# Performance work log

Hardware: AMD Instinct MI355X
Metric: run time of the kernel (lower is better)

Reference implementation:

```python
import jax, jax.numpy as jnp
import numpy as np

NEG = -10000.0
SINK = 16  # first 16 keys are always-attended sink tokens


def setup_inputs() -> dict:
    key = jax.random.key(0)
    k0, k1, k2 = jax.random.split(key, 3)
    B, H, KH, S, D = 1, 16, 4, 2048, 128
    return {
        "query": jax.random.normal(k0, (B, H, S, D), dtype=jnp.float32),
        "key_t": jax.random.normal(k1, (B, KH, S, D), dtype=jnp.float32),
        "value": jax.random.normal(k2, (B, KH, S, D), dtype=jnp.float32),
        "lsh_threshold": jnp.full((KH,), 70.0, dtype=jnp.float32),
        "top_k": 64,
        "window_size": 128,
    }


def reference(query, key_t, value, lsh_threshold, top_k, window_size):
    # query: [B,H,S,D]; key_t/value: [B,KH,S,D] (GQA, QH = H//KH)
    B, H, S, D = query.shape
    KH = key_t.shape[1]
    QH = H // KH
    q = query.reshape(B, KH, QH, S, D)

    # LSH sign-bit matching count. packbits64(x>=0) + (D - xor_popcount) ==
    # number of positions where sign(q)==sign(k) == (D + <sgn(q),sgn(k)>)/2.
    qs = jnp.where(q >= 0, 1.0, -1.0).astype(jnp.float32)
    ksgn = jnp.where(key_t >= 0, 1.0, -1.0).astype(jnp.float32)
    match = (D + jnp.einsum('bkqsd,bkld->bkqsl', qs, ksgn)) * 0.5  # [B,KH,QH,S,S]
    # max over the QH group (dim=2, keepdim) then compare against per-KV-head threshold
    lsh_mask = match.max(axis=2, keepdims=True) > lsh_threshold.reshape(1, KH, 1, 1, 1)

    qi = jnp.arange(S)[:, None]
    ki = jnp.arange(S)[None, :]
    causal = qi >= ki                                             # [S,S]
    window = ((jnp.abs(qi - ki) < window_size) | (ki < SINK)) & causal

    mask = causal & lsh_mask                                      # [B,KH,QH,S,S]

    scale = 1.0 / jnp.sqrt(jnp.asarray(D, jnp.float32))
    scores = jnp.einsum('bkqsd,bkld->bkqsl', q, key_t) * scale    # [B,KH,QH,S,S]
    scores = jnp.where(jnp.logical_not(mask) & jnp.logical_not(window), NEG, scores)

    # long-term candidates: exclude the local window, then take top_k per query row
    scores_lt = jnp.where(window, NEG, scores)
    _, idx = jax.lax.top_k(scores_lt, top_k)                      # [B,KH,QH,S,top_k]
    topk_mask = jnp.put_along_axis(
        jnp.zeros(scores.shape, dtype=bool), idx, True, axis=-1, inplace=False)

    both = window | topk_mask
    probs = jax.nn.softmax(jnp.where(both, scores, NEG), axis=-1)
    out = jnp.einsum('bkqsl,bkld->bskqd', probs, value)           # [B,S,KH,QH,D]
    return out.reshape(B, S, H * D)
```

## Files before the change

### kernel.cpp

```cpp
#include <hip/hip_runtime.h>

#define S_LEN   2048
#define D_DIM   128
#define KH_N    4
#define QH_N    4
#define H_N     (KH_N * QH_N)
#define SINK_N  16
#define MAXW    160
#define MAXC    1904
#define MAXT    2048
#define NREG    16
#define CHUNK   512
#define MAXSEL  208
#define PLANE32 676

typedef __attribute__((ext_vector_type(8))) _Float16 f16x8;
typedef __attribute__((ext_vector_type(2))) _Float16 f16x2;
typedef __attribute__((ext_vector_type(4))) float f32x4;

__device__ __forceinline__ void lds_fence() {
  asm volatile("s_waitcnt lgkmcnt(0)" ::: "memory");
}
__device__ __forceinline__ unsigned short f2h(float f) {
  _Float16 h = (_Float16)f;
  return __builtin_bit_cast(unsigned short, h);
}
__device__ __forceinline__ unsigned int pkrtz_u32(float a, float b) {
  return __builtin_bit_cast(unsigned int, __builtin_amdgcn_cvt_pkrtz(a, b));
}
__device__ __forceinline__ unsigned int pack_okey16(float a, float b) {
  unsigned int u = pkrtz_u32(a, b);
  unsigned int t = (u >> 15) & 0x00010001u;
  return u ^ ((t * 0x7FFFu) | 0x80008000u);
}
__device__ __forceinline__ float okinv16(unsigned int k) {
  unsigned short bits = (k & 0x8000u) ? (unsigned short)(k & 0x7FFFu)
                                      : (unsigned short)(~k & 0xFFFFu);
  return (float)__builtin_bit_cast(_Float16, bits);
}

__global__ __launch_bounds__(256) void pack_kernel(
    const float* __restrict__ k, const float* __restrict__ v,
    unsigned long long* __restrict__ signs,
    unsigned short* __restrict__ kf16, unsigned int* __restrict__ vf16) {
  const int wid  = (blockIdx.x * 256 + threadIdx.x) >> 6;
  const int lane = threadIdx.x & 63;
  const int rbase = wid * 4;
  const int KROWS = KH_N * S_LEN;

  if (rbase < KROWS) {
    const float* src = k + (size_t)rbase * D_DIM;
    float a[4], b[4];
#pragma unroll
    for (int r = 0; r < 4; r++) {
      a[r] = src[r * D_DIM + lane];
      b[r] = src[r * D_DIM + 64 + lane];
    }
#pragma unroll
    for (int r = 0; r < 4; r++) {
      unsigned long long b0 = __ballot(a[r] >= 0.0f);
      unsigned long long b1 = __ballot(b[r] >= 0.0f);
      if (lane == 0) {
        signs[(size_t)(rbase + r) * 2]     = b0;
        signs[(size_t)(rbase + r) * 2 + 1] = b1;
      }
      unsigned short* rb = kf16 + (size_t)(rbase + r) * 128;
      rb[lane]      = f2h(a[r]);
      rb[64 + lane] = f2h(b[r]);
    }
  } else {
    int vr = rbase - KROWS;
    const float* src = v + (size_t)vr * D_DIM;
    float2 f2[4];
#pragma unroll
    for (int r = 0; r < 4; r++)
      f2[r] = *(const float2*)(src + r * D_DIM + lane * 2);
#pragma unroll
    for (int r = 0; r < 4; r++) {
      unsigned int pk = (unsigned int)f2h(f2[r].x) |
                        ((unsigned int)f2h(f2[r].y) << 16);
      vf16[(size_t)(vr + r) * 64 + lane] = pk;
    }
  }
}

__global__ __launch_bounds__(256, 5) void attn_kernel(
    const float* __restrict__ query, const float* __restrict__ thr,
    const int* __restrict__ p_topk, const int* __restrict__ p_wsz,
    const unsigned long long* __restrict__ signs,
    const unsigned short* __restrict__ kf16,
    const unsigned int* __restrict__ vf16,
    float* __restrict__ out) {
  const int xcd  = blockIdx.x & 7;
  const int kh   = xcd >> 1;
  const int s    = (S_LEN - 1) - (((blockIdx.x >> 3) << 1) | (xcd & 1));
  const int tid  = threadIdx.x;
  const int lane = tid & 63;
  const int qh   = tid >> 6;
  const int col  = lane & 15;
  const int quad = lane >> 4;

  __shared__ __align__(16) unsigned int buf[QH_N * PLANE32];
  __shared__ __align__(16) unsigned short q_f16[QH_N][136];
  __shared__ unsigned short idx_sh[MAXT];
  __shared__ unsigned long long qs_sh[QH_N][2];
  __shared__ int ncand_sh;

  const int   topk   = *p_topk;
  const int   wsz    = *p_wsz;
  const float thresh = thr[kh];
  const float scale  = 0.088388347648318447f;

  {
    int h0 = tid >> 7, d = tid & 127;
    float f0 = query[((size_t)(kh * QH_N + h0) * S_LEN + s) * D_DIM + d];
    float f1 = query[((size_t)(kh * QH_N + h0 + 2) * S_LEN + s) * D_DIM + d];
    unsigned long long b0 = __ballot(f0 >= 0.0f);
    unsigned long long b1 = __ballot(f1 >= 0.0f);
    if (lane == 0) {
      qs_sh[qh >> 1][qh & 1] = b0;
      qs_sh[2 + (qh >> 1)][qh & 1] = b1;
    }
    q_f16[h0][d]     = f2h(f0 * scale);
    q_f16[h0 + 2][d] = f2h(f1 * scale);
  }
  if (tid == 0) ncand_sh = 0;

  int wlo = s - (wsz - 1); if (wlo < 0) wlo = 0;
  int nsink = wlo < SINK_N ? wlo : SINK_N;
  int nw = nsink + (s - wlo + 1);
  if (nw > MAXW) nw = MAXW;
  for (int e = tid; e < nw; e += 256)
    idx_sh[e] = (unsigned short)(e < nsink ? e : wlo + (e - nsink));
  __syncthreads();

  unsigned long long qs0[QH_N], qs1[QH_N];
#pragma unroll
  for (int h = 0; h < QH_N; h++) { qs0[h] = qs_sh[h][0]; qs1[h] = qs_sh[h][1]; }
  const unsigned long long* ksg = signs + (size_t)kh * S_LEN * 2;
  int lt_hi = s - wsz;
  for (int l0 = SINK_N; l0 <= lt_hi; l0 += 256) {
    int l = l0 + tid;
    bool match = false;
    if (l <= lt_hi) {
      ulonglong2 kk = *(const ulonglong2*)(ksg + 2 * l);
      int best = 0;
#pragma unroll
      for (int h = 0; h < QH_N; h++) {
        int m = 128 - __popcll(qs0[h] ^ kk.x) - __popcll(qs1[h] ^ kk.y);
        best = best > m ? best : m;
      }
      match = ((float)best > thresh);
    }
    unsigned long long m = __ballot(match);
    if (m) {
      int base = 0;
      if (lane == 0) base = atomicAdd(&ncand_sh, __popcll(m));
      base = __shfl(base, 0);
      if (match) {
        int pos = base + __popcll(m & ((1ull << lane) - 1ull));
        if (pos < MAXC) idx_sh[nw + pos] = (unsigned short)l;
      }
    }
  }
  __syncthreads();
  int nc = ncand_sh < MAXC ? ncand_sh : MAXC;
  int ntot = nw + nc;
  int ntot_pad = (ntot + 15) & ~15;
  for (int i = ntot + tid; i < ntot_pad; i += 256) idx_sh[i] = 0;
  __syncthreads();

  f16x8 bfrag[4];
  f16x8 bzero = {0, 0, 0, 0, 0, 0, 0, 0};
#pragma unroll
  for (int ks = 0; ks < 4; ks++)
    bfrag[ks] = (col < 4) ? *(const f16x8*)&q_f16[col][ks * 32 + quad * 8] : bzero;

  const unsigned short* kf_h = kf16 + ((size_t)kh << 11) * 128;
  unsigned int creg[NREG];
#pragma unroll
  for (int i = 0; i < NREG; i++) creg[i] = 0u;

  for (int cb = 0; cb < 4; cb++) {
    int cbase = cb * CHUNK;
    int chunk_n = ntot_pad - cbase;
    if (chunk_n <= 0) break;
    if (chunk_n > CHUNK) chunk_n = CHUNK;
    int ntiles = chunk_n >> 4;
    for (int t = qh; t < ntiles; t += QH_N) {
      int tb = cbase + t * 16;
      int krow = idx_sh[tb + col];
      const unsigned char* ab =
          (const unsigned char*)(kf_h + (size_t)krow * 128) + quad * 16;
      f16x8 a0 = *(const f16x8*)(ab + 0);
      f16x8 a1 = *(const f16x8*)(ab + 64);
      f16x8 a2 = *(const f16x8*)(ab + 128);
      f16x8 a3 = *(const f16x8*)(ab + 192);
      f32x4 acc = {0.f, 0.f, 0.f, 0.f};
      acc = __builtin_amdgcn_mfma_f32_16x16x32_f16(a0, bfrag[0], acc, 0, 0, 0);
      acc = __builtin_amdgcn_mfma_f32_16x16x32_f16(a1, bfrag[1], acc, 0, 0, 0);
      acc = __builtin_amdgcn_mfma_f32_16x16x32_f16(a2, bfrag[2], acc, 0, 0, 0);
      acc = __builtin_amdgcn_mfma_f32_16x16x32_f16(a3, bfrag[3], acc, 0, 0, 0);
      if (col < 4) {
        unsigned int k01 = pack_okey16(acc[0], acc[1]);
        unsigned int k23 = pack_okey16(acc[2], acc[3]);
        int off = ((tb - cbase) >> 1) + quad * 2;
        buf[col * PLANE32 + off]     = k01;
        buf[col * PLANE32 + off + 1] = k23;
      }
    }
    __syncthreads();
#pragma unroll
    for (int j = 0; j < 4; j++) {
      int m = j * 64 + lane;
      if (2 * m < chunk_n) creg[cb * 4 + j] = buf[qh * PLANE32 + m];
    }
    __syncthreads();
  }
  const int imax = (ntot + 127) >> 7;

  unsigned int*       histw = &buf[qh * PLANE32];
  unsigned long long* selq  = (unsigned long long*)&buf[qh * PLANE32 + 256];

  unsigned int mx16 = 0;
#pragma unroll
  for (int i = 0; i < NREG; i++) {
    if (i >= imax) break;
    unsigned int u = creg[i];
    int e0 = i * 128 + 2 * lane;
    unsigned int h0 = u & 0xFFFFu, h1 = u >> 16;
    if (e0 < ntot && h0 > mx16) mx16 = h0;
    if (e0 + 1 < ntot && h1 > mx16) mx16 = h1;
  }
#pragma unroll
  for (int off = 32; off > 0; off >>= 1) {
    unsigned int t = __shfl_down(mx16, off);
    mx16 = t > mx16 ? t : mx16;
  }
  mx16 = __shfl(mx16, 0);
  const float mxf = okinv16(mx16);

  bool selAll = (nc <= topk);
  unsigned int tkey = 0;
  bool useTie = false;
  int l_cut = S_LEN;
  if (!selAll) {
    unsigned int prefix = 0;
    int want = topk;
    for (int pass = 0; pass < 2; pass++) {
      int sh = 8 - pass * 8;
#pragma unroll
      for (int j = 0; j < 4; j++) histw[lane * 4 + j] = 0;
      lds_fence();
#pragma unroll
      for (int i = 0; i < NREG; i++) {
        if (i >= imax) break;
        unsigned int u = creg[i];
        int e0 = i * 128 + 2 * lane;
#pragma unroll
        for (int h = 0; h < 2; h++) {
          int e = e0 + h;
          if (e >= nw && e < ntot) {
            unsigned int key = h ? (u >> 16) : (u & 0xFFFFu);
            bool match = (pass == 0) || ((key >> 8) == prefix);
            if (match) atomicAdd(&histw[(key >> sh) & 255u], 1u);
          }
        }
      }
      lds_fence();
      unsigned int c0 = histw[lane * 4 + 0];
      unsigned int c1 = histw[lane * 4 + 1];
      unsigned int c2 = histw[lane * 4 + 2];
      unsigned int c3 = histw[lane * 4 + 3];
      unsigned int S3 = c3, S2 = c2 + S3, S1 = c1 + S2, S0 = c0 + S1;
      unsigned int tot = S0;
      unsigned int suf = tot;
#pragma unroll
      for (int off = 1; off < 64; off <<= 1) {
        unsigned int t = __shfl_down(suf, off);
        if (lane + off < 64) suf += t;
      }
      unsigned long long mk = __ballot(suf >= (unsigned int)want);
      int L = 63 - __clzll(mk);
      unsigned int se = suf - tot;
      unsigned int s3 = S3 + se, s2 = S2 + se, s1 = S1 + se, s0 = S0 + se;
      int j; unsigned int above;
      unsigned int w = (unsigned int)want;
      if (s3 >= w)      { j = 3; above = s3 - c3; }
      else if (s2 >= w) { j = 2; above = s2 - c2; }
      else if (s1 >= w) { j = 1; above = s1 - c1; }
      else              { j = 0; above = s0 - c0; }
      int d_me = (lane << 2) | j;
      int wp_me = want - (int)above;
      int digit = __shfl(d_me, L);
      want = __shfl(wp_me, L);
      prefix = (prefix << 8) | (unsigned int)digit;
    }
    tkey = prefix;
    int cgt = 0, ceq = 0;
#pragma unroll
    for (int i = 0; i < NREG; i++) {
      if (i >= imax) break;
      unsigned int u = creg[i];
      int e0 = i * 128 + 2 * lane;
#pragma unroll
      for (int h = 0; h < 2; h++) {
        int e = e0 + h;
        if (e >= nw && e < ntot) {
          unsigned int key = h ? (u >> 16) : (u & 0xFFFFu);
          cgt += (key > tkey);
          ceq += (key == tkey);
        }
      }
    }
#pragma unroll
    for (int off = 32; off > 0; off >>= 1) {
      cgt += __shfl_down(cgt, off);
      ceq += __shfl_down(ceq, off);
    }
    cgt = __shfl(cgt, 0); ceq = __shfl(ceq, 0);
    int rem = topk - cgt;
    if (ceq > rem) {
      useTie = true;
      int lo = 0, hi = S_LEN - 1;
      while (lo < hi) {
        int mid = (lo + hi) >> 1;
        int cn = 0;
#pragma unroll
        for (int i = 0; i < NREG; i++) {
          if (i >= imax) break;
          unsigned int u = creg[i];
          int e0 = i * 128 + 2 * lane;
#pragma unroll
          for (int h = 0; h < 2; h++) {
            int e = e0 + h;
            if (e >= nw && e < ntot) {
              unsigned int key = h ? (u >> 16) : (u & 0xFFFFu);
              cn += (key == tkey && (int)idx_sh[e] <= mid);
            }
          }
        }
#pragma unroll
        for (int off = 32; off > 0; off >>= 1) cn += __shfl_down(cn, off);
        cn = __shfl(cn, 0);
        if (cn >= rem) hi = mid; else lo = mid + 1;
      }
      l_cut = lo;
    }
  }

  float sum = 0.0f;
  int bse = 0;
#pragma unroll
  for (int i = 0; i < NREG; i++) {
    if (i >= imax) break;
    unsigned int u = creg[i];
    int e0 = i * 128 + 2 * lane;
#pragma unroll
    for (int h = 0; h < 2; h++) {
      int e = e0 + h;
      bool act = false;
      float p = 0.f;
      if (e < ntot) {
        unsigned int key = h ? (u >> 16) : (u & 0xFFFFu);
        bool inc = (e < nw) || selAll;
        if (!inc)
          inc = (key > tkey) ||
                (key == tkey && (!useTie || (int)idx_sh[e] <= l_cut));
        if (inc) { act = true; p = __expf(okinv16(key) - mxf); sum += p; }
      }
      unsigned long long m = __ballot(act);
      if (act) {
        int pi = bse + __popcll(m & ((1ull << lane) - 1ull));
        selq[pi] = ((unsigned long long)idx_sh[e] << 32) |
                   (unsigned long long)__float_as_uint(p);
      }
      bse += (int)__popcll(m);
    }
  }
#pragma unroll
  for (int off = 32; off > 0; off >>= 1) sum += __shfl_down(sum, off);
  sum = __shfl(sum, 0);
  float rinv = 1.0f / sum;

  int nsel = bse;
  int nsel8 = (nsel + 7) & ~7;
  if (lane < nsel8 - nsel) selq[nsel + lane] = 0ull;
  lds_fence();

  const int sub = lane & 15;
  const int quarter = lane >> 4;
  float av[8] = {0.f, 0.f, 0.f, 0.f, 0.f, 0.f, 0.f, 0.f};
  const uint4* vb4 = (const uint4*)(vf16 + ((size_t)kh << 11) * 64);
  for (int e = 0; e < nsel8; e += 8) {
    ulonglong2 sp = *(const ulonglong2*)&selq[e + 2 * quarter];
    float p0 = __uint_as_float((unsigned int)sp.x);
    float p1 = __uint_as_float((unsigned int)sp.y);
    int l0 = (int)(sp.x >> 32), l1 = (int)(sp.y >> 32);
    f16x2 ph = __builtin_bit_cast(f16x2, pkrtz_u32(p0, p1));
    uint4 v0 = vb4[(size_t)l0 * 16 + sub];
    uint4 v1 = vb4[(size_t)l1 * 16 + sub];
#define DOT2(comp, i0, i1)                                                   \
    {                                                                        \
      unsigned int lo_ = __builtin_amdgcn_perm(v1.comp, v0.comp, 0x05040100u); \
      unsigned int hi_ = __builtin_amdgcn_perm(v1.comp, v0.comp, 0x07060302u); \
      av[i0] = __builtin_amdgcn_fdot2(__builtin_bit_cast(f16x2, lo_), ph,    \
                                      av[i0], false);                        \
      av[i1] = __builtin_amdgcn_fdot2(__builtin_bit_cast(f16x2, hi_), ph,    \
                                      av[i1], false);                        \
    }
    DOT2(x, 0, 1) DOT2(y, 2, 3) DOT2(z, 4, 5) DOT2(w, 6, 7)
#undef DOT2
  }
#pragma unroll
  for (int d = 0; d < 8; d++) {
    av[d] += __shfl_xor(av[d], 16);
    av[d] += __shfl_xor(av[d], 32);
  }
  if (lane < 16) {
    size_t o = (size_t)s * (H_N * D_DIM) + (size_t)(kh * QH_N + qh) * D_DIM
             + (size_t)sub * 8;
    f32x4 r0 = {av[0] * rinv, av[1] * rinv, av[2] * rinv, av[3] * rinv};
    f32x4 r1 = {av[4] * rinv, av[5] * rinv, av[6] * rinv, av[7] * rinv};
    __builtin_nontemporal_store(r0, (f32x4*)(out + o));
    __builtin_nontemporal_store(r1, (f32x4*)(out + o + 4));
  }
}

extern "C" void kernel_launch(void* const* d_in, const int* in_sizes, int n_in,
                              void* d_out, int out_size, void* d_ws, size_t ws_size,
                              hipStream_t stream) {
  const float* query = (const float*)d_in[0];
  const float* key   = (const float*)d_in[1];
  const float* value = (const float*)d_in[2];
  const float* thr   = (const float*)d_in[3];
  const int* p_topk  = (const int*)d_in[4];
  const int* p_wsz   = (const int*)d_in[5];
  float* out = (float*)d_out;

  char* ws = (char*)d_ws;
  unsigned long long* signs = (unsigned long long*)ws;
  unsigned short* kf16 = (unsigned short*)(ws + (size_t)KH_N * S_LEN * 16);
  unsigned int* vf16 = (unsigned int*)(ws + (size_t)KH_N * S_LEN * 16
                                          + (size_t)KH_N * S_LEN * 256);

  pack_kernel<<<1024, 256, 0, stream>>>(key, value, signs, kf16, vf16);

  attn_kernel<<<KH_N * S_LEN, 256, 0, stream>>>(
      query, thr, p_topk, p_wsz, signs, kf16, vf16, out);
}
```

Measured before the change: 252.5 us.

## Software-pipeline gathered K and V loads; vectorize histogram LDS ops; pack reductions

```diff
diff --git a/kernel.cpp b/kernel.cpp
--- a/kernel.cpp
+++ b/kernel.cpp
@@ -187,26 +187,45 @@
     if (chunk_n <= 0) break;
     if (chunk_n > CHUNK) chunk_n = CHUNK;
     int ntiles = chunk_n >> 4;
-    for (int t = qh; t < ntiles; t += QH_N) {
-      int tb = cbase + t * 16;
-      int krow = idx_sh[tb + col];
+    int t = qh;
+    if (t < ntiles) {
       const unsigned char* ab =
-          (const unsigned char*)(kf_h + (size_t)krow * 128) + quad * 16;
+          (const unsigned char*)(kf_h +
+                                 (size_t)idx_sh[cbase + t * 16 + col] * 128) +
+          quad * 16;
       f16x8 a0 = *(const f16x8*)(ab + 0);
       f16x8 a1 = *(const f16x8*)(ab + 64);
       f16x8 a2 = *(const f16x8*)(ab + 128);
       f16x8 a3 = *(const f16x8*)(ab + 192);
-      f32x4 acc = {0.f, 0.f, 0.f, 0.f};
-      acc = __builtin_amdgcn_mfma_f32_16x16x32_f16(a0, bfrag[0], acc, 0, 0, 0);
-      acc = __builtin_amdgcn_mfma_f32_16x16x32_f16(a1, bfrag[1], acc, 0, 0, 0);
-      acc = __builtin_amdgcn_mfma_f32_16x16x32_f16(a2, bfrag[2], acc, 0, 0, 0);
-      acc = __builtin_amdgcn_mfma_f32_16x16x32_f16(a3, bfrag[3], acc, 0, 0, 0);
-      if (col < 4) {
-        unsigned int k01 = pack_okey16(acc[0], acc[1]);
-        unsigned int k23 = pack_okey16(acc[2], acc[3]);
-        int off = ((tb - cbase) >> 1) + quad * 2;
-        buf[col * PLANE32 + off]     = k01;
-        buf[col * PLANE32 + off + 1] = k23;
+      while (true) {
+        int tn = t + QH_N;
+        bool more = (tn < ntiles);
+        f16x8 n0, n1, n2, n3;
+        if (more) {
+          const unsigned char* ab2 =
+              (const unsigned char*)(kf_h +
+                                     (size_t)idx_sh[cbase + tn * 16 + col] * 128) +
+              quad * 16;
+          n0 = *(const f16x8*)(ab2 + 0);
+          n1 = *(const f16x8*)(ab2 + 64);
+          n2 = *(const f16x8*)(ab2 + 128);
+          n3 = *(const f16x8*)(ab2 + 192);
+        }
+        f32x4 acc = {0.f, 0.f, 0.f, 0.f};
+        acc = __builtin_amdgcn_mfma_f32_16x16x32_f16(a0, bfrag[0], acc, 0, 0, 0);
+        acc = __builtin_amdgcn_mfma_f32_16x16x32_f16(a1, bfrag[1], acc, 0, 0, 0);
+        acc = __builtin_amdgcn_mfma_f32_16x16x32_f16(a2, bfrag[2], acc, 0, 0, 0);
+        acc = __builtin_amdgcn_mfma_f32_16x16x32_f16(a3, bfrag[3], acc, 0, 0, 0);
+        if (col < 4) {
+          unsigned int k01 = pack_okey16(acc[0], acc[1]);
+          unsigned int k23 = pack_okey16(acc[2], acc[3]);
+          int off = t * 8 + quad * 2;
+          buf[col * PLANE32 + off]     = k01;
+          buf[col * PLANE32 + off + 1] = k23;
+        }
+        if (!more) break;
+        a0 = n0; a1 = n1; a2 = n2; a3 = n3;
+        t = tn;
       }
     }
     __syncthreads();
@@ -249,8 +268,10 @@
     int want = topk;
     for (int pass = 0; pass < 2; pass++) {
       int sh = 8 - pass * 8;
-#pragma unroll
-      for (int j = 0; j < 4; j++) histw[lane * 4 + j] = 0;
+      {
+        uint4 z = {0u, 0u, 0u, 0u};
+        *(uint4*)&histw[lane * 4] = z;
+      }
       lds_fence();
 #pragma unroll
       for (int i = 0; i < NREG; i++) {
@@ -268,10 +289,8 @@
         }
       }
       lds_fence();
-      unsigned int c0 = histw[lane * 4 + 0];
-      unsigned int c1 = histw[lane * 4 + 1];
-      unsigned int c2 = histw[lane * 4 + 2];
-      unsigned int c3 = histw[lane * 4 + 3];
+      uint4 cc = *(const uint4*)&histw[lane * 4];
+      unsigned int c0 = cc.x, c1 = cc.y, c2 = cc.z, c3 = cc.w;
       unsigned int S3 = c3, S2 = c2 + S3, S1 = c1 + S2, S0 = c0 + S1;
       unsigned int tot = S0;
       unsigned int suf = tot;
@@ -313,16 +332,15 @@
         }
       }
     }
-#pragma unroll
-    for (int off = 32; off > 0; off >>= 1) {
-      cgt += __shfl_down(cgt, off);
-      ceq += __shfl_down(ceq, off);
-    }
-    cgt = __shfl(cgt, 0); ceq = __shfl(ceq, 0);
+    unsigned int cge = ((unsigned int)cgt << 16) | (unsigned int)ceq;
+#pragma unroll
+    for (int off = 32; off > 0; off >>= 1) cge += __shfl_down(cge, off);
+    cge = __shfl(cge, 0);
+    cgt = (int)(cge >> 16); ceq = (int)(cge & 0xFFFFu);
     int rem = topk - cgt;
     if (ceq > rem) {
       useTie = true;
-      int lo = 0, hi = S_LEN - 1;
+      int lo = SINK_N, hi = lt_hi;
       while (lo < hi) {
         int mid = (lo + hi) >> 1;
         int cn = 0;
@@ -378,10 +396,6 @@
       bse += (int)__popcll(m);
     }
   }
-#pragma unroll
-  for (int off = 32; off > 0; off >>= 1) sum += __shfl_down(sum, off);
-  sum = __shfl(sum, 0);
-  float rinv = 1.0f / sum;
 
   int nsel = bse;
   int nsel8 = (nsel + 7) & ~7;
@@ -390,16 +404,32 @@
 
   const int sub = lane & 15;
   const int quarter = lane >> 4;
+  const uint4* vb4 = (const uint4*)(vf16 + ((size_t)kh << 11) * 64);
+
+  ulonglong2 sp = *(const ulonglong2*)&selq[2 * quarter];
+  uint4 v0 = vb4[(size_t)(int)(sp.x >> 32) * 16 + sub];
+  uint4 v1 = vb4[(size_t)(int)(sp.y >> 32) * 16 + sub];
+
+#pragma unroll
+  for (int off = 32; off > 0; off >>= 1) sum += __shfl_down(sum, off);
+  sum = __shfl(sum, 0);
+  float rinv = 1.0f / sum;
+
   float av[8] = {0.f, 0.f, 0.f, 0.f, 0.f, 0.f, 0.f, 0.f};
-  const uint4* vb4 = (const uint4*)(vf16 + ((size_t)kh << 11) * 64);
-  for (int e = 0; e < nsel8; e += 8) {
-    ulonglong2 sp = *(const ulonglong2*)&selq[e + 2 * quarter];
+  int e = 0;
+  while (true) {
+    int en = e + 8;
+    bool more = (en < nsel8);
+    ulonglong2 spn;
+    uint4 w0, w1;
+    if (more) {
+      spn = *(const ulonglong2*)&selq[en + 2 * quarter];
+      w0 = vb4[(size_t)(int)(spn.x >> 32) * 16 + sub];
+      w1 = vb4[(size_t)(int)(spn.y >> 32) * 16 + sub];
+    }
     float p0 = __uint_as_float((unsigned int)sp.x);
     float p1 = __uint_as_float((unsigned int)sp.y);
-    int l0 = (int)(sp.x >> 32), l1 = (int)(sp.y >> 32);
     f16x2 ph = __builtin_bit_cast(f16x2, pkrtz_u32(p0, p1));
-    uint4 v0 = vb4[(size_t)l0 * 16 + sub];
-    uint4 v1 = vb4[(size_t)l1 * 16 + sub];
 #define DOT2(comp, i0, i1)                                                   \
     {                                                                        \
       unsigned int lo_ = __builtin_amdgcn_perm(v1.comp, v0.comp, 0x05040100u); \
@@ -411,6 +441,8 @@
     }
     DOT2(x, 0, 1) DOT2(y, 2, 3) DOT2(z, 4, 5) DOT2(w, 6, 7)
 #undef DOT2
+    if (!more) break;
+    sp = spn; v0 = w0; v1 = w1; e = en;
   }
 #pragma unroll
   for (int d = 0; d < 8; d++) {
```

After: 275.5 us. 9.1% more time.

## Reuse radix histogram counts for tie handling and double score chunk size

Applied to the files above, without the earlier changes.

```diff
diff --git a/kernel.cpp b/kernel.cpp
--- a/kernel.cpp
+++ b/kernel.cpp
@@ -10,9 +10,10 @@
 #define MAXC    1904
 #define MAXT    2048
 #define NREG    16
-#define CHUNK   512
+#define CHUNK   1024
 #define MAXSEL  208
 #define PLANE32 676
+#define TIECAP  672
 
 typedef __attribute__((ext_vector_type(8))) _Float16 f16x8;
 typedef __attribute__((ext_vector_type(2))) _Float16 f16x2;
@@ -181,7 +182,7 @@
 #pragma unroll
   for (int i = 0; i < NREG; i++) creg[i] = 0u;
 
-  for (int cb = 0; cb < 4; cb++) {
+  for (int cb = 0; cb < 2; cb++) {
     int cbase = cb * CHUNK;
     int chunk_n = ntot_pad - cbase;
     if (chunk_n <= 0) break;
@@ -211,9 +212,9 @@
     }
     __syncthreads();
 #pragma unroll
-    for (int j = 0; j < 4; j++) {
+    for (int j = 0; j < 8; j++) {
       int m = j * 64 + lane;
-      if (2 * m < chunk_n) creg[cb * 4 + j] = buf[qh * PLANE32 + m];
+      if (2 * m < chunk_n) creg[cb * 8 + j] = buf[qh * PLANE32 + m];
     }
     __syncthreads();
   }
@@ -247,10 +248,13 @@
   if (!selAll) {
     unsigned int prefix = 0;
     int want = topk;
+    unsigned int ceq = 0;
     for (int pass = 0; pass < 2; pass++) {
       int sh = 8 - pass * 8;
-#pragma unroll
-      for (int j = 0; j < 4; j++) histw[lane * 4 + j] = 0;
+      {
+        uint4 z = {0u, 0u, 0u, 0u};
+        *(uint4*)&histw[lane * 4] = z;
+      }
       lds_fence();
 #pragma unroll
       for (int i = 0; i < NREG; i++) {
@@ -268,10 +272,8 @@
         }
       }
       lds_fence();
-      unsigned int c0 = histw[lane * 4 + 0];
-      unsigned int c1 = histw[lane * 4 + 1];
-      unsigned int c2 = histw[lane * 4 + 2];
-      unsigned int c3 = histw[lane * 4 + 3];
+      uint4 cc = *(const uint4*)&histw[lane * 4];
+      unsigned int c0 = cc.x, c1 = cc.y, c2 = cc.z, c3 = cc.w;
       unsigned int S3 = c3, S2 = c2 + S3, S1 = c1 + S2, S0 = c0 + S1;
       unsigned int tot = S0;
       unsigned int suf = tot;
@@ -284,48 +286,26 @@
       int L = 63 - __clzll(mk);
       unsigned int se = suf - tot;
       unsigned int s3 = S3 + se, s2 = S2 + se, s1 = S1 + se, s0 = S0 + se;
-      int j; unsigned int above;
+      int j; unsigned int above, csel;
       unsigned int w = (unsigned int)want;
-      if (s3 >= w)      { j = 3; above = s3 - c3; }
-      else if (s2 >= w) { j = 2; above = s2 - c2; }
-      else if (s1 >= w) { j = 1; above = s1 - c1; }
-      else              { j = 0; above = s0 - c0; }
+      if (s3 >= w)      { j = 3; above = s3 - c3; csel = c3; }
+      else if (s2 >= w) { j = 2; above = s2 - c2; csel = c2; }
+      else if (s1 >= w) { j = 1; above = s1 - c1; csel = c1; }
+      else              { j = 0; above = s0 - c0; csel = c0; }
       int d_me = (lane << 2) | j;
       int wp_me = want - (int)above;
       int digit = __shfl(d_me, L);
       want = __shfl(wp_me, L);
+      ceq = (unsigned int)__shfl((int)csel, L);
       prefix = (prefix << 8) | (unsigned int)digit;
     }
     tkey = prefix;
-    int cgt = 0, ceq = 0;
-#pragma unroll
-    for (int i = 0; i < NREG; i++) {
-      if (i >= imax) break;
-      unsigned int u = creg[i];
-      int e0 = i * 128 + 2 * lane;
-#pragma unroll
-      for (int h = 0; h < 2; h++) {
-        int e = e0 + h;
-        if (e >= nw && e < ntot) {
-          unsigned int key = h ? (u >> 16) : (u & 0xFFFFu);
-          cgt += (key > tkey);
-          ceq += (key == tkey);
-        }
-      }
-    }
-#pragma unroll
-    for (int off = 32; off > 0; off >>= 1) {
-      cgt += __shfl_down(cgt, off);
-      ceq += __shfl_down(ceq, off);
-    }
-    cgt = __shfl(cgt, 0); ceq = __shfl(ceq, 0);
-    int rem = topk - cgt;
-    if (ceq > rem) {
+    int rem = want;
+    if ((int)ceq > rem) {
       useTie = true;
-      int lo = 0, hi = S_LEN - 1;
-      while (lo < hi) {
-        int mid = (lo + hi) >> 1;
-        int cn = 0;
+      if ((int)ceq <= TIECAP) {
+        unsigned int* tls = histw;
+        int tb = 0;
 #pragma unroll
         for (int i = 0; i < NREG; i++) {
           if (i >= imax) break;
@@ -334,18 +314,59 @@
 #pragma unroll
           for (int h = 0; h < 2; h++) {
             int e = e0 + h;
+            bool tied = false;
             if (e >= nw && e < ntot) {
               unsigned int key = h ? (u >> 16) : (u & 0xFFFFu);
-              cn += (key == tkey && (int)idx_sh[e] <= mid);
+              tied = (key == tkey);
+            }
+            unsigned long long m = __ballot(tied);
+            if (tied) {
+              int pos = tb + __popcll(m & ((1ull << lane) - 1ull));
+              tls[pos] = (unsigned int)idx_sh[e];
+            }
+            tb += (int)__popcll(m);
+          }
+        }
+        lds_fence();
+        unsigned int lcut = (unsigned int)S_LEN;
+        for (int i = lane; i < (int)ceq; i += 64) {
+          unsigned int v = tls[i];
+          int rank = 0;
+          for (int j2 = 0; j2 < (int)ceq; j2++) rank += (tls[j2] < v);
+          if (rank == rem - 1) lcut = v;
+        }
+#pragma unroll
+        for (int off = 32; off > 0; off >>= 1) {
+          unsigned int t = __shfl_down(lcut, off);
+          lcut = t < lcut ? t : lcut;
+        }
+        l_cut = (int)__shfl((int)lcut, 0);
+      } else {
+        int lo = SINK_N, hi = lt_hi;
+        while (lo < hi) {
+          int mid = (lo + hi) >> 1;
+          int cn = 0;
+#pragma unroll
+          for (int i = 0; i < NREG; i++) {
+            if (i >= imax) break;
+            unsigned int u = creg[i];
+            int e0 = i * 128 + 2 * lane;
+#pragma unroll
+            for (int h = 0; h < 2; h++) {
+              int e = e0 + h;
+              if (e >= nw && e < ntot) {
+                unsigned int key = h ? (u >> 16) : (u & 0xFFFFu);
+                cn += (key == tkey && (int)idx_sh[e] <= mid);
+              }
             }
           }
+#pragma unroll
+          for (int off = 32; off > 0; off >>= 1) cn += __shfl_down(cn, off);
+          cn = __shfl(cn, 0);
+          if (cn >= rem) hi = mid; else lo = mid + 1;
         }
-#pragma unroll
-        for (int off = 32; off > 0; off >>= 1) cn += __shfl_down(cn, off);
-        cn = __shfl(cn, 0);
-        if (cn >= rem) hi = mid; else lo = mid + 1;
-      }
-      l_cut = lo;
+        l_cut = lo;
+      }
     }
   }
 
```

After: 251.2 us. No clear change (-0.5%).
